# Optimization experiments

Measured on AMD Instinct MI355X. Metric: run time of the kernel, lower is better.

Reference implementation:

```python
import jax, jax.numpy as jnp
import numpy as np


def setup_inputs() -> dict:
    N, E, D = 50000, 800000, 64
    key = jax.random.key(0)
    ks = jax.random.split(key, 8)
    s = 1.0 / np.sqrt(2 * D)
    inp = {
        "node_emb": jax.random.normal(ks[0], (N, D), dtype=jnp.float32),
        "edge_index": jax.random.randint(ks[1], (2, E), 0, N, dtype=jnp.int64),
        "W1": jax.random.normal(ks[2], (2 * D, D), dtype=jnp.float32) * s,
        "b1": jnp.zeros((D,), dtype=jnp.float32),
        "W2": jax.random.normal(ks[3], (D, D), dtype=jnp.float32) * (1.0 / np.sqrt(D)),
        "b2": jnp.zeros((D,), dtype=jnp.float32),
        "Wg": jax.random.normal(ks[4], (D, D), dtype=jnp.float32) * (1.0 / np.sqrt(D)),
        "bg": jnp.zeros((D,), dtype=jnp.float32),
    }
    return inp


def reference(node_emb, edge_index, W1, b1, W2, b2, Wg, bg):
    # Gather pairwise embeddings along edges
    src, dst = edge_index[0], edge_index[1]
    pair_emb = jnp.concatenate([node_emb[src], node_emb[dst]], axis=-1)  # [E, 2D]
    # Interaction MLP (dropout in eval mode -> identity)
    h = jax.nn.relu(pair_emb @ W1 + b1)
    interaction = h @ W2 + b2  # [E, D]
    # Sigmoid gate
    gate = jax.nn.sigmoid(interaction @ Wg + bg)
    gated = interaction * gate  # [E, D]
    # Scatter-mean back to source nodes
    N = node_emb.shape[0]
    summed = jax.ops.segment_sum(gated, src, num_segments=N)  # [N, D]
    counts = jax.ops.segment_sum(jnp.ones((src.shape[0],), dtype=gated.dtype), src, num_segments=N)
    pooled = summed / jnp.maximum(counts, 1.0)[:, None]
    return pooled
```

## Files before the change

kernel.cpp:

```cpp
#include <hip/hip_runtime.h>


typedef unsigned short ushort_t;
typedef __attribute__((ext_vector_type(8))) short     bf16x8;
typedef __attribute__((ext_vector_type(8))) unsigned short u16x8;
typedef __attribute__((ext_vector_type(4))) float     f32x4;

constexpr int D        = 64;
constexpr int TILE     = 64;
constexpr int BLOCK    = 256;
constexpr int NFRAG    = 32;
constexpr int SLAB_B   = 4352;
constexpr int PAIR_STR = 136;
constexpr int H_STR    = 72;

static __device__ __forceinline__ ushort_t f2bf(float f) {
    union { float f; unsigned int u; } v; v.f = f;
    const unsigned int r = v.u + 0x7FFFu + ((v.u >> 16) & 1u);
    return (ushort_t)(r >> 16);
}


__global__ void prep_kernel(const float* __restrict__ W1, const float* __restrict__ W2,
                            const float* __restrict__ Wg,
                            const float* __restrict__ b2, const float* __restrict__ bg,
                            const float* __restrict__ emb, const int* __restrict__ ei,
                            ushort_t* __restrict__ wpack, float* __restrict__ bgp,
                            ushort_t* __restrict__ emb_bf, int* __restrict__ cnt,
                            float* __restrict__ summed,
                            int total_emb, int cvt_blocks, int e4blocks, int E) {
    const int bid = blockIdx.x;
    if (bid < 64) {
        const int t = bid * 256 + threadIdx.x;
        const int f = t >> 9;
        const int l = (t >> 3) & 63;
        const int j = t & 7;
        const int k = ((f < 16) ? (f & 3) : ((f - 16) & 1)) * 32 + (l >> 4) * 8 + j;
        const int n = ((f < 16) ? (f >> 2) : (((f & 7)) >> 1)) * 16 + (l & 15);
        float v;
        if (f < 16)      v = W1[k * 64 + n];
        else if (f < 24) v = W2[k * 64 + n];
        else {
            float s = 0.f;
            const float* wr = W2 + k * 64;
#pragma unroll 8
            for (int m = 0; m < 64; ++m) s += wr[m] * Wg[m * 64 + n];
            v = s;
        }
        wpack[t] = f2bf(v);
    } else if (bid < 64 + cvt_blocks) {
        const int idx  = (bid - 64) * 256 + threadIdx.x;
        const int base = idx * 8;
        if (base < total_emb) {
            const float4 a = *(const float4*)(emb + base);
            const float4 b = *(const float4*)(emb + base + 4);
            u16x8 p;
            p[0]=f2bf(a.x); p[1]=f2bf(a.y); p[2]=f2bf(a.z); p[3]=f2bf(a.w);
            p[4]=f2bf(b.x); p[5]=f2bf(b.y); p[6]=f2bf(b.z); p[7]=f2bf(b.w);
            *(u16x8*)(emb_bf + base) = p;
        }
    } else if (bid == 64 + cvt_blocks) {
        const int n = threadIdx.x;
        if (n < 64) {
            float s = bg[n];
#pragma unroll 8
            for (int m = 0; m < 64; ++m) s += b2[m] * Wg[m * 64 + n];
            bgp[n] = s;
        }
    } else if (bid < 65 + cvt_blocks + e4blocks) {
        const int e = ((bid - 65 - cvt_blocks) * 256 + threadIdx.x) * 4;
        if (e + 3 < E) {
            const int4 v = *(const int4*)(ei + e);
            atomicAdd(&cnt[v.x], 1); atomicAdd(&cnt[v.y], 1);
            atomicAdd(&cnt[v.z], 1); atomicAdd(&cnt[v.w], 1);
        } else {
            for (int k = e; k < E; ++k) atomicAdd(&cnt[ei[k]], 1);
        }
    } else {
        const int idx  = (bid - 65 - cvt_blocks - e4blocks) * 256 + threadIdx.x;
        const int base = idx * 4;
        if (base < total_emb)
            *(float4*)(summed + base) = (float4){0.f, 0.f, 0.f, 0.f};
    }
}


__global__ void scan_block(const int* __restrict__ cnt, int* __restrict__ off,
                           int* __restrict__ bsum, int N) {
    __shared__ int s[256];
    const int t = threadIdx.x, i = blockIdx.x * 256 + t;
    const int x = (i < N) ? cnt[i] : 0;
    s[t] = x; __syncthreads();
    for (int d = 1; d < 256; d <<= 1) {
        const int v = (t >= d) ? s[t - d] : 0;
        __syncthreads();
        s[t] += v;
        __syncthreads();
    }
    if (i < N) off[i] = s[t] - x;
    if (t == 255) bsum[blockIdx.x] = s[255];
}

__global__ void scatter_idx(const int* __restrict__ ei, int* __restrict__ off,
                            const int* __restrict__ bsum, unsigned* __restrict__ sorted,
                            int E, int nb) {
    __shared__ int pref[256];
    const int t = threadIdx.x;
    const int x = (t < nb) ? bsum[t] : 0;
    pref[t] = x; __syncthreads();
    for (int d = 1; d < 256; d <<= 1) {
        const int v = (t >= d) ? pref[t - d] : 0;
        __syncthreads();
        pref[t] += v;
        __syncthreads();
    }
    const int e = (blockIdx.x * blockDim.x + t) * 4;
    if (e + 3 < E) {
        const int4 v = *(const int4*)(ei + e);
        const int4 d = *(const int4*)(ei + E + e);
        const int bx = v.x >> 8, by = v.y >> 8, bz = v.z >> 8, bw = v.w >> 8;
        sorted[(bx ? pref[bx - 1] : 0) + atomicAdd(&off[v.x], 1)] =
            ((unsigned)v.x << 16) | (unsigned)d.x;
        sorted[(by ? pref[by - 1] : 0) + atomicAdd(&off[v.y], 1)] =
            ((unsigned)v.y << 16) | (unsigned)d.y;
        sorted[(bz ? pref[bz - 1] : 0) + atomicAdd(&off[v.z], 1)] =
            ((unsigned)v.z << 16) | (unsigned)d.z;
        sorted[(bw ? pref[bw - 1] : 0) + atomicAdd(&off[v.w], 1)] =
            ((unsigned)v.w << 16) | (unsigned)d.w;
    } else {
        for (int k = e; k < E; ++k) {
            const int s = ei[k], b = s >> 8;
            sorted[(b ? pref[b - 1] : 0) + atomicAdd(&off[s], 1)] =
                ((unsigned)s << 16) | (unsigned)ei[E + k];
        }
    }
}


__global__ __launch_bounds__(BLOCK, 8)
void edge_mlp_mfma(const ushort_t* __restrict__ emb_bf,
                   const unsigned* __restrict__ sorted,
                   const ushort_t* __restrict__ wpack,
                   const float* __restrict__ b1, const float* __restrict__ b2,
                   const float* __restrict__ bgp,
                   const int*   __restrict__ cnt,
                   float* __restrict__ summed,
                   int E)
{
    __shared__ char  slab[4][SLAB_B];
    __shared__ int   srcIds[TILE];
    __shared__ float rcS[TILE];

    const int tid = threadIdx.x;

    {
        const int e = tid >> 2, q4 = tid & 3;
        ushort_t* prow = (ushort_t*)&slab[e >> 4][(e & 15) * (PAIR_STR * 2)];
        const int ide = blockIdx.x * TILE + e;
        if (ide < E) {
            const unsigned p = sorted[ide];
            const int s  = (int)(p >> 16);
            const int dn = (int)(p & 0xFFFFu);
            if (q4 == 0) { srcIds[e] = s; rcS[e] = 1.0f / fmaxf((float)cnt[s], 1.0f); }
            const ushort_t* sr = emb_bf + (size_t)s  * D + q4 * 16;
            const ushort_t* dr = emb_bf + (size_t)dn * D + q4 * 16;
            *(u16x8*)&prow[q4 * 16]          = *(const u16x8*)sr;
            *(u16x8*)&prow[q4 * 16 + 8]      = *(const u16x8*)(sr + 8);
            *(u16x8*)&prow[64 + q4 * 16]     = *(const u16x8*)dr;
            *(u16x8*)&prow[64 + q4 * 16 + 8] = *(const u16x8*)(dr + 8);
        } else {
            if (q4 == 0) { srcIds[e] = -1; rcS[e] = 1.0f; }
            const u16x8 z = {0,0,0,0,0,0,0,0};
            *(u16x8*)&prow[q4 * 16]          = z;
            *(u16x8*)&prow[q4 * 16 + 8]      = z;
            *(u16x8*)&prow[64 + q4 * 16]     = z;
            *(u16x8*)&prow[64 + q4 * 16 + 8] = z;
        }
    }

    const int w    = tid >> 6;
    const int ln   = tid & 63;
    const int quad = ln >> 4;
    const int cn   = ln & 15;
    ushort_t* pairW = (ushort_t*)slab[w];
    ushort_t* hW    = (ushort_t*)slab[w];

    f32x4 acc1[4];
#pragma unroll
    for (int nt = 0; nt < 4; ++nt) {
        const float b = b1[nt * 16 + cn];
        acc1[nt] = (f32x4){b, b, b, b};
    }
#pragma unroll
    for (int kc = 0; kc < 4; ++kc) {
        const bf16x8 a = *(const bf16x8*)&pairW[cn * PAIR_STR + kc * 32 + quad * 8];
#pragma unroll
        for (int nt = 0; nt < 4; ++nt) {
            const bf16x8 bf = *(const bf16x8*)(wpack + ((nt * 4 + kc) * 64 + ln) * 8);
            acc1[nt] = __builtin_amdgcn_mfma_f32_16x16x32_bf16(a, bf, acc1[nt], 0, 0, 0);
        }
    }
#pragma unroll
    for (int nt = 0; nt < 4; ++nt)
#pragma unroll
        for (int r = 0; r < 4; ++r)
            hW[(quad * 4 + r) * H_STR + nt * 16 + cn] = f2bf(fmaxf(acc1[nt][r], 0.f));

    f32x4 acc2[4], accg[4];
#pragma unroll
    for (int nt = 0; nt < 4; ++nt) {
        const float b  = b2 [nt * 16 + cn];
        const float bG = bgp[nt * 16 + cn];
        acc2[nt] = (f32x4){b, b, b, b};
        accg[nt] = (f32x4){bG, bG, bG, bG};
    }
#pragma unroll
    for (int kc = 0; kc < 2; ++kc) {
        const bf16x8 a = *(const bf16x8*)&hW[cn * H_STR + kc * 32 + quad * 8];
#pragma unroll
        for (int nt = 0; nt < 4; ++nt) {
            const bf16x8 bf2 = *(const bf16x8*)(wpack + ((16 + nt * 2 + kc) * 64 + ln) * 8);
            const bf16x8 bfg = *(const bf16x8*)(wpack + ((24 + nt * 2 + kc) * 64 + ln) * 8);
            acc2[nt] = __builtin_amdgcn_mfma_f32_16x16x32_bf16(a, bf2, acc2[nt], 0, 0, 0);
            accg[nt] = __builtin_amdgcn_mfma_f32_16x16x32_bf16(a, bfg, accg[nt], 0, 0, 0);
        }
    }

    float g[4][4];
#pragma unroll
    for (int nt = 0; nt < 4; ++nt)
#pragma unroll
        for (int r = 0; r < 4; ++r)
            g[nt][r] = acc2[nt][r] / (1.0f + __expf(-accg[nt][r]));

    {
        const int rbase = 16 * w;
        float part0 = 0.f, part1 = 0.f, part2 = 0.f, part3 = 0.f;
        int   segSrc = srcIds[rbase];
        int   segRow = 0;
#pragma unroll
        for (int i = 0; i < 16; ++i) {
            const int s = srcIds[rbase + i];
            if (s != segSrc) {
                if (segSrc >= 0) {
                    float t0 = part0, t1 = part1, t2 = part2, t3 = part3;
                    t0 += __shfl_xor(t0, 16); t0 += __shfl_xor(t0, 32);
                    t1 += __shfl_xor(t1, 16); t1 += __shfl_xor(t1, 32);
                    t2 += __shfl_xor(t2, 16); t2 += __shfl_xor(t2, 32);
                    t3 += __shfl_xor(t3, 16); t3 += __shfl_xor(t3, 32);
                    const float tot = (quad < 2) ? (quad == 0 ? t0 : t1)
                                                 : (quad == 2 ? t2 : t3);
                    unsafeAtomicAdd(&summed[(size_t)segSrc * D + ln],
                                    tot * rcS[rbase + segRow]);
                }
                part0 = part1 = part2 = part3 = 0.f;
                segSrc = s;
                segRow = i;
            }
            if ((i >> 2) == quad) {
                part0 += g[0][i & 3];
                part1 += g[1][i & 3];
                part2 += g[2][i & 3];
                part3 += g[3][i & 3];
            }
        }
        if (segSrc >= 0) {
            float t0 = part0, t1 = part1, t2 = part2, t3 = part3;
            t0 += __shfl_xor(t0, 16); t0 += __shfl_xor(t0, 32);
            t1 += __shfl_xor(t1, 16); t1 += __shfl_xor(t1, 32);
            t2 += __shfl_xor(t2, 16); t2 += __shfl_xor(t2, 32);
            t3 += __shfl_xor(t3, 16); t3 += __shfl_xor(t3, 32);
            const float tot = (quad < 2) ? (quad == 0 ? t0 : t1)
                                         : (quad == 2 ? t2 : t3);
            unsafeAtomicAdd(&summed[(size_t)segSrc * D + ln],
                            tot * rcS[rbase + segRow]);
        }
    }
}

extern "C" void kernel_launch(void* const* d_in, const int* in_sizes, int n_in,
                              void* d_out, int out_size, void* d_ws, size_t ws_size,
                              hipStream_t stream) {
    const float* node_emb   = (const float*)d_in[0];
    const int*   edge_index = (const int*)d_in[1];
    const float* W1 = (const float*)d_in[2];
    const float* b1 = (const float*)d_in[3];
    const float* W2 = (const float*)d_in[4];
    const float* b2 = (const float*)d_in[5];
    const float* Wg = (const float*)d_in[6];
    const float* bg = (const float*)d_in[7];

    const int N = in_sizes[0] / D;
    const int E = in_sizes[1] / 2;
    const int total_emb = N * D;

    int* cnt    = (int*)d_ws;
    int* off    = cnt + N;
    int* bsum   = off + N;
    unsigned* sorted = (unsigned*)(bsum + 256);
    float* bgp  = (float*)(sorted + E);
    ushort_t* wpack  = (ushort_t*)(bgp + 64);
    ushort_t* emb_bf = wpack + NFRAG * 512;

    float* summed = (float*)d_out;

    hipMemsetAsync(cnt, 0, sizeof(int) * (size_t)N, stream);

    const int cvt_blocks = (total_emb / 8 + 255) / 256;
    const int e4blocks   = ((E + 3) / 4 + 255) / 256;
    const int zblocks    = (total_emb / 4 + 255) / 256;
    prep_kernel<<<64 + cvt_blocks + 1 + e4blocks + zblocks, 256, 0, stream>>>(
        W1, W2, Wg, b2, bg, node_emb, edge_index,
        wpack, bgp, emb_bf, cnt, summed, total_emb, cvt_blocks, e4blocks, E);

    const int nblocks = (N + 255) / 256;
    scan_block <<<nblocks, 256, 0, stream>>>(cnt, off, bsum, N);
    scatter_idx<<<e4blocks, 256, 0, stream>>>(edge_index, off, bsum, sorted, E, nblocks);

    const int ntiles = (E + TILE - 1) / TILE;
    edge_mlp_mfma<<<ntiles, BLOCK, 0, stream>>>(emb_bf, sorted, wpack,
                                                b1, b2, bgp, cnt, summed, E);
}
```

Measured before the change: 245.3 us.

## Fuse all stages into one persistent kernel with software grid barriers

Merges the prep, counting, scan, scatter and edge-MLP kernels into a single persistent kernel of 1024 blocks. The stages are separated by atomic-counter grid barriers, and the MFMA tiles are processed in a grid-stride loop. The aim is to remove kernel launch gaps and the separate memset of the counts. The cost is spin-wait barriers, which deadlock if not all blocks are co-resident, reduced parallelism in the fill phases, and lower occupancy from launch_bounds 4.

```diff
diff --git a/kernel.cpp b/kernel.cpp
--- a/kernel.cpp
+++ b/kernel.cpp
@@ -9,6 +9,7 @@
 constexpr int D        = 64;
 constexpr int TILE     = 64;
 constexpr int BLOCK    = 256;
+constexpr int NBLK     = 1024;
 constexpr int NFRAG    = 32;
 constexpr int SLAB_B   = 4352;
 constexpr int PAIR_STR = 136;
@@ -20,18 +21,39 @@
     return (ushort_t)(r >> 16);
 }
 
-
-__global__ void prep_kernel(const float* __restrict__ W1, const float* __restrict__ W2,
-                            const float* __restrict__ Wg,
-                            const float* __restrict__ b2, const float* __restrict__ bg,
-                            const float* __restrict__ emb, const int* __restrict__ ei,
-                            ushort_t* __restrict__ wpack, float* __restrict__ bgp,
-                            ushort_t* __restrict__ emb_bf, int* __restrict__ cnt,
-                            float* __restrict__ summed,
-                            int total_emb, int cvt_blocks, int e4blocks, int E) {
+static __device__ __forceinline__ void grid_sync(unsigned* bar, unsigned target) {
+    __syncthreads();
+    if (threadIdx.x == 0) {
+        __hip_atomic_fetch_add(bar, 1u, __ATOMIC_ACQ_REL, __HIP_MEMORY_SCOPE_AGENT);
+        while (__hip_atomic_load(bar, __ATOMIC_ACQUIRE, __HIP_MEMORY_SCOPE_AGENT) < target)
+            __builtin_amdgcn_s_sleep(8);
+    }
+    __syncthreads();
+}
+
+__global__ __launch_bounds__(BLOCK, 4)
+void uber_kernel(const float* __restrict__ W1, const float* __restrict__ W2,
+                 const float* __restrict__ Wg, const float* __restrict__ pb1,
+                 const float* __restrict__ pb2, const float* __restrict__ pbg,
+                 const float* __restrict__ emb, const int* __restrict__ ei,
+                 unsigned* __restrict__ bar, int* __restrict__ cnt,
+                 int* __restrict__ off, int* __restrict__ bsum,
+                 unsigned* __restrict__ sorted, float* __restrict__ bgp,
+                 ushort_t* __restrict__ wpack, ushort_t* __restrict__ emb_bf,
+                 float* __restrict__ summed,
+                 int N, int E, int total_emb, int ntiles, int nsb)
+{
+    __shared__ char  slab[4][SLAB_B];
+    __shared__ int   si[256];
+    __shared__ int   srcIds[TILE];
+    __shared__ float rcS[TILE];
+
+    const int tid = threadIdx.x;
     const int bid = blockIdx.x;
-    if (bid < 64) {
-        const int t = bid * 256 + threadIdx.x;
+    const int gid = bid * BLOCK + tid;
+    constexpr int G = NBLK * BLOCK;
+
+    for (int t = gid; t < NFRAG * 512; t += G) {
         const int f = t >> 9;
         const int l = (t >> 3) & 63;
         const int j = t & 7;
@@ -48,27 +70,30 @@
             v = s;
         }
         wpack[t] = f2bf(v);
-    } else if (bid < 64 + cvt_blocks) {
-        const int idx  = (bid - 64) * 256 + threadIdx.x;
-        const int base = idx * 8;
-        if (base < total_emb) {
-            const float4 a = *(const float4*)(emb + base);
-            const float4 b = *(const float4*)(emb + base + 4);
-            u16x8 p;
-            p[0]=f2bf(a.x); p[1]=f2bf(a.y); p[2]=f2bf(a.z); p[3]=f2bf(a.w);
-            p[4]=f2bf(b.x); p[5]=f2bf(b.y); p[6]=f2bf(b.z); p[7]=f2bf(b.w);
-            *(u16x8*)(emb_bf + base) = p;
-        }
-    } else if (bid == 64 + cvt_blocks) {
-        const int n = threadIdx.x;
-        if (n < 64) {
-            float s = bg[n];
+    }
+    if (gid < 64) {
+        float s = pbg[gid];
 #pragma unroll 8
-            for (int m = 0; m < 64; ++m) s += b2[m] * Wg[m * 64 + n];
-            bgp[n] = s;
-        }
-    } else if (bid < 65 + cvt_blocks + e4blocks) {
-        const int e = ((bid - 65 - cvt_blocks) * 256 + threadIdx.x) * 4;
+        for (int m = 0; m < 64; ++m) s += pb2[m] * Wg[m * 64 + gid];
+        bgp[gid] = s;
+    }
+    for (int i = gid; i < N; i += G) cnt[i] = 0;
+    for (int i = gid; i * 8 < total_emb; i += G) {
+        const int base = i * 8;
+        const float4 a = *(const float4*)(emb + base);
+        const float4 b = *(const float4*)(emb + base + 4);
+        u16x8 p;
+        p[0]=f2bf(a.x); p[1]=f2bf(a.y); p[2]=f2bf(a.z); p[3]=f2bf(a.w);
+        p[4]=f2bf(b.x); p[5]=f2bf(b.y); p[6]=f2bf(b.z); p[7]=f2bf(b.w);
+        *(u16x8*)(emb_bf + base) = p;
+    }
+    for (int i = gid; i * 4 < total_emb; i += G)
+        *(float4*)(summed + i * 4) = (float4){0.f, 0.f, 0.f, 0.f};
+
+    grid_sync(bar, 1u * NBLK);
+
+    for (int i = gid; i * 4 < E; i += G) {
+        const int e = i * 4;
         if (e + 3 < E) {
             const int4 v = *(const int4*)(ei + e);
             atomicAdd(&cnt[v.x], 1); atomicAdd(&cnt[v.y], 1);
@@ -76,107 +101,59 @@
         } else {
             for (int k = e; k < E; ++k) atomicAdd(&cnt[ei[k]], 1);
         }
-    } else {
-        const int idx  = (bid - 65 - cvt_blocks - e4blocks) * 256 + threadIdx.x;
-        const int base = idx * 4;
-        if (base < total_emb)
-            *(float4*)(summed + base) = (float4){0.f, 0.f, 0.f, 0.f};
-    }
-}
-
-
-__global__ void scan_block(const int* __restrict__ cnt, int* __restrict__ off,
-                           int* __restrict__ bsum, int N) {
-    __shared__ int s[256];
-    const int t = threadIdx.x, i = blockIdx.x * 256 + t;
-    const int x = (i < N) ? cnt[i] : 0;
-    s[t] = x; __syncthreads();
-    for (int d = 1; d < 256; d <<= 1) {
-        const int v = (t >= d) ? s[t - d] : 0;
-        __syncthreads();
-        s[t] += v;
-        __syncthreads();
-    }
-    if (i < N) off[i] = s[t] - x;
-    if (t == 255) bsum[blockIdx.x] = s[255];
-}
-
-__global__ void scatter_idx(const int* __restrict__ ei, int* __restrict__ off,
-                            const int* __restrict__ bsum, unsigned* __restrict__ sorted,
-                            int E, int nb) {
-    __shared__ int pref[256];
-    const int t = threadIdx.x;
-    const int x = (t < nb) ? bsum[t] : 0;
-    pref[t] = x; __syncthreads();
-    for (int d = 1; d < 256; d <<= 1) {
-        const int v = (t >= d) ? pref[t - d] : 0;
-        __syncthreads();
-        pref[t] += v;
-        __syncthreads();
-    }
-    const int e = (blockIdx.x * blockDim.x + t) * 4;
-    if (e + 3 < E) {
-        const int4 v = *(const int4*)(ei + e);
-        const int4 d = *(const int4*)(ei + E + e);
-        const int bx = v.x >> 8, by = v.y >> 8, bz = v.z >> 8, bw = v.w >> 8;
-        sorted[(bx ? pref[bx - 1] : 0) + atomicAdd(&off[v.x], 1)] =
-            ((unsigned)v.x << 16) | (unsigned)d.x;
-        sorted[(by ? pref[by - 1] : 0) + atomicAdd(&off[v.y], 1)] =
-            ((unsigned)v.y << 16) | (unsigned)d.y;
-        sorted[(bz ? pref[bz - 1] : 0) + atomicAdd(&off[v.z], 1)] =
-            ((unsigned)v.z << 16) | (unsigned)d.z;
-        sorted[(bw ? pref[bw - 1] : 0) + atomicAdd(&off[v.w], 1)] =
-            ((unsigned)v.w << 16) | (unsigned)d.w;
-    } else {
-        for (int k = e; k < E; ++k) {
-            const int s = ei[k], b = s >> 8;
-            sorted[(b ? pref[b - 1] : 0) + atomicAdd(&off[s], 1)] =
-                ((unsigned)s << 16) | (unsigned)ei[E + k];
-        }
-    }
-}
-
-
-__global__ __launch_bounds__(BLOCK, 8)
-void edge_mlp_mfma(const ushort_t* __restrict__ emb_bf,
-                   const unsigned* __restrict__ sorted,
-                   const ushort_t* __restrict__ wpack,
-                   const float* __restrict__ b1, const float* __restrict__ b2,
-                   const float* __restrict__ bgp,
-                   const int*   __restrict__ cnt,
-                   float* __restrict__ summed,
-                   int E)
-{
-    __shared__ char  slab[4][SLAB_B];
-    __shared__ int   srcIds[TILE];
-    __shared__ float rcS[TILE];
-
-    const int tid = threadIdx.x;
-
-    {
-        const int e = tid >> 2, q4 = tid & 3;
-        ushort_t* prow = (ushort_t*)&slab[e >> 4][(e & 15) * (PAIR_STR * 2)];
-        const int ide = blockIdx.x * TILE + e;
-        if (ide < E) {
-            const unsigned p = sorted[ide];
-            const int s  = (int)(p >> 16);
-            const int dn = (int)(p & 0xFFFFu);
-            if (q4 == 0) { srcIds[e] = s; rcS[e] = 1.0f / fmaxf((float)cnt[s], 1.0f); }
-            const ushort_t* sr = emb_bf + (size_t)s  * D + q4 * 16;
-            const ushort_t* dr = emb_bf + (size_t)dn * D + q4 * 16;
-            *(u16x8*)&prow[q4 * 16]          = *(const u16x8*)sr;
-            *(u16x8*)&prow[q4 * 16 + 8]      = *(const u16x8*)(sr + 8);
-            *(u16x8*)&prow[64 + q4 * 16]     = *(const u16x8*)dr;
-            *(u16x8*)&prow[64 + q4 * 16 + 8] = *(const u16x8*)(dr + 8);
+    }
+    grid_sync(bar, 2u * NBLK);
+
+    if (bid < nsb) {
+        const int i = bid * 256 + tid;
+        const int x = (i < N) ? cnt[i] : 0;
+        si[tid] = x; __syncthreads();
+        for (int d = 1; d < 256; d <<= 1) {
+            const int v = (tid >= d) ? si[tid - d] : 0;
+            __syncthreads();
+            si[tid] += v;
+            __syncthreads();
+        }
+        if (i < N) off[i] = si[tid] - x;
+        if (tid == 255) bsum[bid] = si[255];
+    }
+    grid_sync(bar, 3u * NBLK);
+
+    if (bid == 0) {
+        const int x = (tid < nsb) ? bsum[tid] : 0;
+        si[tid] = x; __syncthreads();
+        for (int d = 1; d < 256; d <<= 1) {
+            const int v = (tid >= d) ? si[tid - d] : 0;
+            __syncthreads();
+            si[tid] += v;
+            __syncthreads();
+        }
+        if (tid < nsb) bsum[tid] = si[tid] - x;
+    }
+    grid_sync(bar, 4u * NBLK);
+
+    for (int i = gid; i * 4 < E; i += G) {
+        const int e = i * 4;
+        if (e + 3 < E) {
+            const int4 v  = *(const int4*)(ei + e);
+            const int4 d4 = *(const int4*)(ei + E + e);
+            sorted[bsum[v.x >> 8] + atomicAdd(&off[v.x], 1)] =
+                ((unsigned)v.x << 16) | (unsigned)d4.x;
+            sorted[bsum[v.y >> 8] + atomicAdd(&off[v.y], 1)] =
+                ((unsigned)v.y << 16) | (unsigned)d4.y;
+            sorted[bsum[v.z >> 8] + atomicAdd(&off[v.z], 1)] =
+                ((unsigned)v.z << 16) | (unsigned)d4.z;
+            sorted[bsum[v.w >> 8] + atomicAdd(&off[v.w], 1)] =
+                ((unsigned)v.w << 16) | (unsigned)d4.w;
         } else {
-            if (q4 == 0) { srcIds[e] = -1; rcS[e] = 1.0f; }
-            const u16x8 z = {0,0,0,0,0,0,0,0};
-            *(u16x8*)&prow[q4 * 16]          = z;
-            *(u16x8*)&prow[q4 * 16 + 8]      = z;
-            *(u16x8*)&prow[64 + q4 * 16]     = z;
-            *(u16x8*)&prow[64 + q4 * 16 + 8] = z;
-        }
-    }
+            for (int k = e; k < E; ++k) {
+                const int s = ei[k];
+                sorted[bsum[s >> 8] + atomicAdd(&off[s], 1)] =
+                    ((unsigned)s << 16) | (unsigned)ei[E + k];
+            }
+        }
+    }
+    grid_sync(bar, 5u * NBLK);
 
     const int w    = tid >> 6;
     const int ln   = tid & 63;
@@ -185,95 +162,122 @@
     ushort_t* pairW = (ushort_t*)slab[w];
     ushort_t* hW    = (ushort_t*)slab[w];
 
-    f32x4 acc1[4];
-#pragma unroll
-    for (int nt = 0; nt < 4; ++nt) {
-        const float b = b1[nt * 16 + cn];
-        acc1[nt] = (f32x4){b, b, b, b};
-    }
-#pragma unroll
-    for (int kc = 0; kc < 4; ++kc) {
-        const bf16x8 a = *(const bf16x8*)&pairW[cn * PAIR_STR + kc * 32 + quad * 8];
+    for (int tile = bid; tile < ntiles; tile += NBLK) {
+        {
+            const int e = tid >> 2, q4 = tid & 3;
+            ushort_t* prow = (ushort_t*)&slab[e >> 4][(e & 15) * (PAIR_STR * 2)];
+            const int ide = tile * TILE + e;
+            if (ide < E) {
+                const unsigned p = sorted[ide];
+                const int s  = (int)(p >> 16);
+                const int dn = (int)(p & 0xFFFFu);
+                if (q4 == 0) { srcIds[e] = s; rcS[e] = 1.0f / fmaxf((float)cnt[s], 1.0f); }
+                const ushort_t* sr = emb_bf + (size_t)s  * D + q4 * 16;
+                const ushort_t* dr = emb_bf + (size_t)dn * D + q4 * 16;
+                *(u16x8*)&prow[q4 * 16]          = *(const u16x8*)sr;
+                *(u16x8*)&prow[q4 * 16 + 8]      = *(const u16x8*)(sr + 8);
+                *(u16x8*)&prow[64 + q4 * 16]     = *(const u16x8*)dr;
+                *(u16x8*)&prow[64 + q4 * 16 + 8] = *(const u16x8*)(dr + 8);
+            } else {
+                if (q4 == 0) { srcIds[e] = -1; rcS[e] = 1.0f; }
+                const u16x8 z = {0,0,0,0,0,0,0,0};
+                *(u16x8*)&prow[q4 * 16]          = z;
+                *(u16x8*)&prow[q4 * 16 + 8]      = z;
+                *(u16x8*)&prow[64 + q4 * 16]     = z;
+                *(u16x8*)&prow[64 + q4 * 16 + 8] = z;
+            }
+        }
+
+        f32x4 acc1[4];
 #pragma unroll
         for (int nt = 0; nt < 4; ++nt) {
-            const bf16x8 bf = *(const bf16x8*)(wpack + ((nt * 4 + kc) * 64 + ln) * 8);
-            acc1[nt] = __builtin_amdgcn_mfma_f32_16x16x32_bf16(a, bf, acc1[nt], 0, 0, 0);
-        }
-    }
-#pragma unroll
-    for (int nt = 0; nt < 4; ++nt)
-#pragma unroll
-        for (int r = 0; r < 4; ++r)
-            hW[(quad * 4 + r) * H_STR + nt * 16 + cn] = f2bf(fmaxf(acc1[nt][r], 0.f));
-
-    f32x4 acc2[4], accg[4];
-#pragma unroll
-    for (int nt = 0; nt < 4; ++nt) {
-        const float b  = b2 [nt * 16 + cn];
-        const float bG = bgp[nt * 16 + cn];
-        acc2[nt] = (f32x4){b, b, b, b};
-        accg[nt] = (f32x4){bG, bG, bG, bG};
-    }
-#pragma unroll
-    for (int kc = 0; kc < 2; ++kc) {
-        const bf16x8 a = *(const bf16x8*)&hW[cn * H_STR + kc * 32 + quad * 8];
+            const float b = pb1[nt * 16 + cn];
+            acc1[nt] = (f32x4){b, b, b, b};
+        }
+#pragma unroll
+        for (int kc = 0; kc < 4; ++kc) {
+            const bf16x8 a = *(const bf16x8*)&pairW[cn * PAIR_STR + kc * 32 + quad * 8];
+#pragma unroll
+            for (int nt = 0; nt < 4; ++nt) {
+                const bf16x8 bf = *(const bf16x8*)(wpack + ((nt * 4 + kc) * 64 + ln) * 8);
+                acc1[nt] = __builtin_amdgcn_mfma_f32_16x16x32_bf16(a, bf, acc1[nt], 0, 0, 0);
+            }
+        }
+#pragma unroll
+        for (int nt = 0; nt < 4; ++nt)
+#pragma unroll
+            for (int r = 0; r < 4; ++r)
+                hW[(quad * 4 + r) * H_STR + nt * 16 + cn] = f2bf(fmaxf(acc1[nt][r], 0.f));
+
+        f32x4 acc2[4], accg[4];
 #pragma unroll
         for (int nt = 0; nt < 4; ++nt) {
-            const bf16x8 bf2 = *(const bf16x8*)(wpack + ((16 + nt * 2 + kc) * 64 + ln) * 8);
-            const bf16x8 bfg = *(const bf16x8*)(wpack + ((24 + nt * 2 + kc) * 64 + ln) * 8);
-            acc2[nt] = __builtin_amdgcn_mfma_f32_16x16x32_bf16(a, bf2, acc2[nt], 0, 0, 0);
-            accg[nt] = __builtin_amdgcn_mfma_f32_16x16x32_bf16(a, bfg, accg[nt], 0, 0, 0);
-        }
-    }
-
-    float g[4][4];
-#pragma unroll
-    for (int nt = 0; nt < 4; ++nt)
-#pragma unroll
-        for (int r = 0; r < 4; ++r)
-            g[nt][r] = acc2[nt][r] / (1.0f + __expf(-accg[nt][r]));
-
-    {
-        const int rbase = 16 * w;
-        float part0 = 0.f, part1 = 0.f, part2 = 0.f, part3 = 0.f;
-        int   segSrc = srcIds[rbase];
-        int   segRow = 0;
-#pragma unroll
-        for (int i = 0; i < 16; ++i) {
-            const int s = srcIds[rbase + i];
-            if (s != segSrc) {
-                if (segSrc >= 0) {
-                    float t0 = part0, t1 = part1, t2 = part2, t3 = part3;
-                    t0 += __shfl_xor(t0, 16); t0 += __shfl_xor(t0, 32);
-                    t1 += __shfl_xor(t1, 16); t1 += __shfl_xor(t1, 32);
-                    t2 += __shfl_xor(t2, 16); t2 += __shfl_xor(t2, 32);
-                    t3 += __shfl_xor(t3, 16); t3 += __shfl_xor(t3, 32);
-                    const float tot = (quad < 2) ? (quad == 0 ? t0 : t1)
-                                                 : (quad == 2 ? t2 : t3);
-                    unsafeAtomicAdd(&summed[(size_t)segSrc * D + ln],
-                                    tot * rcS[rbase + segRow]);
+            const float b  = pb2[nt * 16 + cn];
+            const float bG = bgp[nt * 16 + cn];
+            acc2[nt] = (f32x4){b, b, b, b};
+            accg[nt] = (f32x4){bG, bG, bG, bG};
+        }
+#pragma unroll
+        for (int kc = 0; kc < 2; ++kc) {
+            const bf16x8 a = *(const bf16x8*)&hW[cn * H_STR + kc * 32 + quad * 8];
+#pragma unroll
+            for (int nt = 0; nt < 4; ++nt) {
+                const bf16x8 bf2 = *(const bf16x8*)(wpack + ((16 + nt * 2 + kc) * 64 + ln) * 8);
+                const bf16x8 bfg = *(const bf16x8*)(wpack + ((24 + nt * 2 + kc) * 64 + ln) * 8);
+                acc2[nt] = __builtin_amdgcn_mfma_f32_16x16x32_bf16(a, bf2, acc2[nt], 0, 0, 0);
+                accg[nt] = __builtin_amdgcn_mfma_f32_16x16x32_bf16(a, bfg, accg[nt], 0, 0, 0);
+            }
+        }
+
+        float g[4][4];
+#pragma unroll
+        for (int nt = 0; nt < 4; ++nt)
+#pragma unroll
+            for (int r = 0; r < 4; ++r)
+                g[nt][r] = acc2[nt][r] / (1.0f + __expf(-accg[nt][r]));
+
+        {
+            const int rbase = 16 * w;
+            float part0 = 0.f, part1 = 0.f, part2 = 0.f, part3 = 0.f;
+            int   segSrc = srcIds[rbase];
+            int   segRow = 0;
+#pragma unroll
+            for (int i = 0; i < 16; ++i) {
+                const int s = srcIds[rbase + i];
+                if (s != segSrc) {
+                    if (segSrc >= 0) {
+                        float t0 = part0, t1 = part1, t2 = part2, t3 = part3;
+                        t0 += __shfl_xor(t0, 16); t0 += __shfl_xor(t0, 32);
+                        t1 += __shfl_xor(t1, 16); t1 += __shfl_xor(t1, 32);
+                        t2 += __shfl_xor(t2, 16); t2 += __shfl_xor(t2, 32);
+                        t3 += __shfl_xor(t3, 16); t3 += __shfl_xor(t3, 32);
+                        const float tot = (quad < 2) ? (quad == 0 ? t0 : t1)
+                                                     : (quad == 2 ? t2 : t3);
+                        unsafeAtomicAdd(&summed[(size_t)segSrc * D + ln],
+                                        tot * rcS[rbase + segRow]);
+                    }
+                    part0 = part1 = part2 = part3 = 0.f;
+                    segSrc = s;
+                    segRow = i;
                 }
-                part0 = part1 = part2 = part3 = 0.f;
-                segSrc = s;
-                segRow = i;
-            }
-            if ((i >> 2) == quad) {
-                part0 += g[0][i & 3];
-                part1 += g[1][i & 3];
-                part2 += g[2][i & 3];
-                part3 += g[3][i & 3];
-            }
-        }
-        if (segSrc >= 0) {
-            float t0 = part0, t1 = part1, t2 = part2, t3 = part3;
-            t0 += __shfl_xor(t0, 16); t0 += __shfl_xor(t0, 32);
-            t1 += __shfl_xor(t1, 16); t1 += __shfl_xor(t1, 32);
-            t2 += __shfl_xor(t2, 16); t2 += __shfl_xor(t2, 32);
-            t3 += __shfl_xor(t3, 16); t3 += __shfl_xor(t3, 32);
-            const float tot = (quad < 2) ? (quad == 0 ? t0 : t1)
-                                         : (quad == 2 ? t2 : t3);
-            unsafeAtomicAdd(&summed[(size_t)segSrc * D + ln],
-                            tot * rcS[rbase + segRow]);
+                if ((i >> 2) == quad) {
+                    part0 += g[0][i & 3];
+                    part1 += g[1][i & 3];
+                    part2 += g[2][i & 3];
+                    part3 += g[3][i & 3];
+                }
+            }
+            if (segSrc >= 0) {
+                float t0 = part0, t1 = part1, t2 = part2, t3 = part3;
+                t0 += __shfl_xor(t0, 16); t0 += __shfl_xor(t0, 32);
+                t1 += __shfl_xor(t1, 16); t1 += __shfl_xor(t1, 32);
+                t2 += __shfl_xor(t2, 16); t2 += __shfl_xor(t2, 32);
+                t3 += __shfl_xor(t3, 16); t3 += __shfl_xor(t3, 32);
+                const float tot = (quad < 2) ? (quad == 0 ? t0 : t1)
+                                             : (quad == 2 ? t2 : t3);
+                unsafeAtomicAdd(&summed[(size_t)segSrc * D + ln],
+                                tot * rcS[rbase + segRow]);
+            }
         }
     }
 }
@@ -294,30 +298,23 @@
     const int E = in_sizes[1] / 2;
     const int total_emb = N * D;
 
-    int* cnt    = (int*)d_ws;
+    unsigned* bar = (unsigned*)d_ws;
+    int* cnt    = (int*)d_ws + 16;
     int* off    = cnt + N;
     int* bsum   = off + N;
-    unsigned* sorted = (unsigned*)(bsum + 256);
+    unsigned* sorted = (unsigned*)(bsum + 240);
     float* bgp  = (float*)(sorted + E);
     ushort_t* wpack  = (ushort_t*)(bgp + 64);
     ushort_t* emb_bf = wpack + NFRAG * 512;
 
     float* summed = (float*)d_out;
 
-    hipMemsetAsync(cnt, 0, sizeof(int) * (size_t)N, stream);
-
-    const int cvt_blocks = (total_emb / 8 + 255) / 256;
-    const int e4blocks   = ((E + 3) / 4 + 255) / 256;
-    const int zblocks    = (total_emb / 4 + 255) / 256;
-    prep_kernel<<<64 + cvt_blocks + 1 + e4blocks + zblocks, 256, 0, stream>>>(
-        W1, W2, Wg, b2, bg, node_emb, edge_index,
-        wpack, bgp, emb_bf, cnt, summed, total_emb, cvt_blocks, e4blocks, E);
-
-    const int nblocks = (N + 255) / 256;
-    scan_block <<<nblocks, 256, 0, stream>>>(cnt, off, bsum, N);
-    scatter_idx<<<e4blocks, 256, 0, stream>>>(edge_index, off, bsum, sorted, E, nblocks);
+    hipMemsetAsync(bar, 0, 64, stream);
 
     const int ntiles = (E + TILE - 1) / TILE;
-    edge_mlp_mfma<<<ntiles, BLOCK, 0, stream>>>(emb_bf, sorted, wpack,
-                                                b1, b2, bgp, cnt, summed, E);
+    const int nsb    = (N + 255) / 256;
+    uber_kernel<<<NBLK, BLOCK, 0, stream>>>(
+        W1, W2, Wg, b1, b2, bg, node_emb, edge_index,
+        bar, cnt, off, bsum, sorted, bgp, wpack, emb_bf,
+        summed, N, E, total_emb, ntiles, nsb);
 }
```

New measurement: 850.0 us. +246.6%, slower.

## Make edge MLP kernel persistent with register prefetch of next tile's gathers

Applied to the files above, without the earlier changes.

The edge MLP kernel becomes a grid-stride persistent kernel with a fixed grid of 1536 blocks, each looping over many 64-edge tiles. Inside the loop, the sorted-index lookup and bf16 embedding gathers for the next tile are issued into registers after the first MFMA stage, so their global-memory latency overlaps the remaining matmuls and the scatter of the current tile. Occupancy hint drops from 8 to 6 blocks to make room for the prefetch registers. The trade-off is fewer resident waves to hide latency, plus possible tail imbalance from the fixed grid.

```diff
diff --git a/kernel.cpp b/kernel.cpp
--- a/kernel.cpp
+++ b/kernel.cpp
@@ -9,6 +9,7 @@
 constexpr int D        = 64;
 constexpr int TILE     = 64;
 constexpr int BLOCK    = 256;
+constexpr int NBLK_M   = 1536;
 constexpr int NFRAG    = 32;
 constexpr int SLAB_B   = 4352;
 constexpr int PAIR_STR = 136;
@@ -116,28 +117,28 @@
     }
     const int e = (blockIdx.x * blockDim.x + t) * 4;
     if (e + 3 < E) {
-        const int4 v = *(const int4*)(ei + e);
-        const int4 d = *(const int4*)(ei + E + e);
+        const int4 v  = *(const int4*)(ei + e);
+        const int4 d4 = *(const int4*)(ei + E + e);
         const int bx = v.x >> 8, by = v.y >> 8, bz = v.z >> 8, bw = v.w >> 8;
         sorted[(bx ? pref[bx - 1] : 0) + atomicAdd(&off[v.x], 1)] =
-            ((unsigned)v.x << 16) | (unsigned)d.x;
+            ((unsigned)v.x << 16) | (unsigned)d4.x;
         sorted[(by ? pref[by - 1] : 0) + atomicAdd(&off[v.y], 1)] =
-            ((unsigned)v.y << 16) | (unsigned)d.y;
+            ((unsigned)v.y << 16) | (unsigned)d4.y;
         sorted[(bz ? pref[bz - 1] : 0) + atomicAdd(&off[v.z], 1)] =
-            ((unsigned)v.z << 16) | (unsigned)d.z;
+            ((unsigned)v.z << 16) | (unsigned)d4.z;
         sorted[(bw ? pref[bw - 1] : 0) + atomicAdd(&off[v.w], 1)] =
-            ((unsigned)v.w << 16) | (unsigned)d.w;
+            ((unsigned)v.w << 16) | (unsigned)d4.w;
     } else {
         for (int k = e; k < E; ++k) {
-            const int s = ei[k], b = s >> 8;
-            sorted[(b ? pref[b - 1] : 0) + atomicAdd(&off[s], 1)] =
+            const int s = ei[k], c = s >> 8;
+            sorted[(c ? pref[c - 1] : 0) + atomicAdd(&off[s], 1)] =
                 ((unsigned)s << 16) | (unsigned)ei[E + k];
         }
     }
 }
 
 
-__global__ __launch_bounds__(BLOCK, 8)
+__global__ __launch_bounds__(BLOCK, 6)
 void edge_mlp_mfma(const ushort_t* __restrict__ emb_bf,
                    const unsigned* __restrict__ sorted,
                    const ushort_t* __restrict__ wpack,
@@ -145,135 +146,159 @@
                    const float* __restrict__ bgp,
                    const int*   __restrict__ cnt,
                    float* __restrict__ summed,
-                   int E)
+                   int E, int ntiles)
 {
     __shared__ char  slab[4][SLAB_B];
     __shared__ int   srcIds[TILE];
     __shared__ float rcS[TILE];
 
-    const int tid = threadIdx.x;
-
-    {
-        const int e = tid >> 2, q4 = tid & 3;
-        ushort_t* prow = (ushort_t*)&slab[e >> 4][(e & 15) * (PAIR_STR * 2)];
-        const int ide = blockIdx.x * TILE + e;
-        if (ide < E) {
-            const unsigned p = sorted[ide];
-            const int s  = (int)(p >> 16);
-            const int dn = (int)(p & 0xFFFFu);
-            if (q4 == 0) { srcIds[e] = s; rcS[e] = 1.0f / fmaxf((float)cnt[s], 1.0f); }
-            const ushort_t* sr = emb_bf + (size_t)s  * D + q4 * 16;
-            const ushort_t* dr = emb_bf + (size_t)dn * D + q4 * 16;
-            *(u16x8*)&prow[q4 * 16]          = *(const u16x8*)sr;
-            *(u16x8*)&prow[q4 * 16 + 8]      = *(const u16x8*)(sr + 8);
-            *(u16x8*)&prow[64 + q4 * 16]     = *(const u16x8*)dr;
-            *(u16x8*)&prow[64 + q4 * 16 + 8] = *(const u16x8*)(dr + 8);
-        } else {
-            if (q4 == 0) { srcIds[e] = -1; rcS[e] = 1.0f; }
-            const u16x8 z = {0,0,0,0,0,0,0,0};
-            *(u16x8*)&prow[q4 * 16]          = z;
-            *(u16x8*)&prow[q4 * 16 + 8]      = z;
-            *(u16x8*)&prow[64 + q4 * 16]     = z;
-            *(u16x8*)&prow[64 + q4 * 16 + 8] = z;
-        }
-    }
-
+    const int tid  = threadIdx.x;
+    const int e    = tid >> 2, q4 = tid & 3;
     const int w    = tid >> 6;
     const int ln   = tid & 63;
     const int quad = ln >> 4;
     const int cn   = ln & 15;
+    ushort_t* prow  = (ushort_t*)&slab[e >> 4][(e & 15) * (PAIR_STR * 2)];
     ushort_t* pairW = (ushort_t*)slab[w];
     ushort_t* hW    = (ushort_t*)slab[w];
 
-    f32x4 acc1[4];
-#pragma unroll
-    for (int nt = 0; nt < 4; ++nt) {
-        const float b = b1[nt * 16 + cn];
-        acc1[nt] = (f32x4){b, b, b, b};
-    }
-#pragma unroll
-    for (int kc = 0; kc < 4; ++kc) {
-        const bf16x8 a = *(const bf16x8*)&pairW[cn * PAIR_STR + kc * 32 + quad * 8];
+    const u16x8 z = {0,0,0,0,0,0,0,0};
+    u16x8 r0 = z, r1 = z, r2 = z, r3 = z;
+    int   ps  = -1;
+    float prc = 1.0f;
+
+    {
+        const int ide = blockIdx.x * TILE + e;
+        if (blockIdx.x < ntiles && ide < E) {
+            const unsigned p = sorted[ide];
+            const int s  = (int)(p >> 16);
+            const int dn = (int)(p & 0xFFFFu);
+            ps = s;
+            if (q4 == 0) prc = 1.0f / fmaxf((float)cnt[s], 1.0f);
+            const ushort_t* sr = emb_bf + (size_t)s  * D + q4 * 16;
+            const ushort_t* dr = emb_bf + (size_t)dn * D + q4 * 16;
+            r0 = *(const u16x8*)sr; r1 = *(const u16x8*)(sr + 8);
+            r2 = *(const u16x8*)dr; r3 = *(const u16x8*)(dr + 8);
+        }
+    }
+
+    for (int tile = blockIdx.x; tile < ntiles; tile += gridDim.x) {
+        *(u16x8*)&prow[q4 * 16]          = r0;
+        *(u16x8*)&prow[q4 * 16 + 8]      = r1;
+        *(u16x8*)&prow[64 + q4 * 16]     = r2;
+        *(u16x8*)&prow[64 + q4 * 16 + 8] = r3;
+        if (q4 == 0) { srcIds[e] = ps; rcS[e] = prc; }
+
+        f32x4 acc1[4];
 #pragma unroll
         for (int nt = 0; nt < 4; ++nt) {
-            const bf16x8 bf = *(const bf16x8*)(wpack + ((nt * 4 + kc) * 64 + ln) * 8);
-            acc1[nt] = __builtin_amdgcn_mfma_f32_16x16x32_bf16(a, bf, acc1[nt], 0, 0, 0);
-        }
-    }
-#pragma unroll
-    for (int nt = 0; nt < 4; ++nt)
-#pragma unroll
-        for (int r = 0; r < 4; ++r)
-            hW[(quad * 4 + r) * H_STR + nt * 16 + cn] = f2bf(fmaxf(acc1[nt][r], 0.f));
-
-    f32x4 acc2[4], accg[4];
-#pragma unroll
-    for (int nt = 0; nt < 4; ++nt) {
-        const float b  = b2 [nt * 16 + cn];
-        const float bG = bgp[nt * 16 + cn];
-        acc2[nt] = (f32x4){b, b, b, b};
-        accg[nt] = (f32x4){bG, bG, bG, bG};
-    }
-#pragma unroll
-    for (int kc = 0; kc < 2; ++kc) {
-        const bf16x8 a = *(const bf16x8*)&hW[cn * H_STR + kc * 32 + quad * 8];
+            const float b = b1[nt * 16 + cn];
+            acc1[nt] = (f32x4){b, b, b, b};
+        }
+#pragma unroll
+        for (int kc = 0; kc < 4; ++kc) {
+            const bf16x8 a = *(const bf16x8*)&pairW[cn * PAIR_STR + kc * 32 + quad * 8];
+#pragma unroll
+            for (int nt = 0; nt < 4; ++nt) {
+                const bf16x8 bf = *(const bf16x8*)(wpack + ((nt * 4 + kc) * 64 + ln) * 8);
+                acc1[nt] = __builtin_amdgcn_mfma_f32_16x16x32_bf16(a, bf, acc1[nt], 0, 0, 0);
+            }
+        }
+
+        {
+            const int t2  = tile + (int)gridDim.x;
+            const int ide = t2 * TILE + e;
+            if (t2 < ntiles && ide < E) {
+                const unsigned p = sorted[ide];
+                const int s  = (int)(p >> 16);
+                const int dn = (int)(p & 0xFFFFu);
+                ps = s;
+                if (q4 == 0) prc = 1.0f / fmaxf((float)cnt[s], 1.0f);
+                const ushort_t* sr = emb_bf + (size_t)s  * D + q4 * 16;
+                const ushort_t* dr = emb_bf + (size_t)dn * D + q4 * 16;
+                r0 = *(const u16x8*)sr; r1 = *(const u16x8*)(sr + 8);
+                r2 = *(const u16x8*)dr; r3 = *(const u16x8*)(dr + 8);
+            } else {
+                ps = -1; prc = 1.0f;
+                r0 = z; r1 = z; r2 = z; r3 = z;
+            }
+        }
+
+#pragma unroll
+        for (int nt = 0; nt < 4; ++nt)
+#pragma unroll
+            for (int r = 0; r < 4; ++r)
+                hW[(quad * 4 + r) * H_STR + nt * 16 + cn] = f2bf(fmaxf(acc1[nt][r], 0.f));
+
+        f32x4 acc2[4], accg[4];
 #pragma unroll
         for (int nt = 0; nt < 4; ++nt) {
-            const bf16x8 bf2 = *(const bf16x8*)(wpack + ((16 + nt * 2 + kc) * 64 + ln) * 8);
-            const bf16x8 bfg = *(const bf16x8*)(wpack + ((24 + nt * 2 + kc) * 64 + ln) * 8);
-            acc2[nt] = __builtin_amdgcn_mfma_f32_16x16x32_bf16(a, bf2, acc2[nt], 0, 0, 0);
-            accg[nt] = __builtin_amdgcn_mfma_f32_16x16x32_bf16(a, bfg, accg[nt], 0, 0, 0);
-        }
-    }
-
-    float g[4][4];
-#pragma unroll
-    for (int nt = 0; nt < 4; ++nt)
-#pragma unroll
-        for (int r = 0; r < 4; ++r)
-            g[nt][r] = acc2[nt][r] / (1.0f + __expf(-accg[nt][r]));
-
-    {
-        const int rbase = 16 * w;
-        float part0 = 0.f, part1 = 0.f, part2 = 0.f, part3 = 0.f;
-        int   segSrc = srcIds[rbase];
-        int   segRow = 0;
-#pragma unroll
-        for (int i = 0; i < 16; ++i) {
-            const int s = srcIds[rbase + i];
-            if (s != segSrc) {
-                if (segSrc >= 0) {
-                    float t0 = part0, t1 = part1, t2 = part2, t3 = part3;
-                    t0 += __shfl_xor(t0, 16); t0 += __shfl_xor(t0, 32);
-                    t1 += __shfl_xor(t1, 16); t1 += __shfl_xor(t1, 32);
-                    t2 += __shfl_xor(t2, 16); t2 += __shfl_xor(t2, 32);
-                    t3 += __shfl_xor(t3, 16); t3 += __shfl_xor(t3, 32);
-                    const float tot = (quad < 2) ? (quad == 0 ? t0 : t1)
-                                                 : (quad == 2 ? t2 : t3);
-                    unsafeAtomicAdd(&summed[(size_t)segSrc * D + ln],
-                                    tot * rcS[rbase + segRow]);
+            const float b  = b2 [nt * 16 + cn];
+            const float bG = bgp[nt * 16 + cn];
+            acc2[nt] = (f32x4){b, b, b, b};
+            accg[nt] = (f32x4){bG, bG, bG, bG};
+        }
+#pragma unroll
+        for (int kc = 0; kc < 2; ++kc) {
+            const bf16x8 a = *(const bf16x8*)&hW[cn * H_STR + kc * 32 + quad * 8];
+#pragma unroll
+            for (int nt = 0; nt < 4; ++nt) {
+                const bf16x8 bf2 = *(const bf16x8*)(wpack + ((16 + nt * 2 + kc) * 64 + ln) * 8);
+                const bf16x8 bfg = *(const bf16x8*)(wpack + ((24 + nt * 2 + kc) * 64 + ln) * 8);
+                acc2[nt] = __builtin_amdgcn_mfma_f32_16x16x32_bf16(a, bf2, acc2[nt], 0, 0, 0);
+                accg[nt] = __builtin_amdgcn_mfma_f32_16x16x32_bf16(a, bfg, accg[nt], 0, 0, 0);
+            }
+        }
+
+        float g[4][4];
+#pragma unroll
+        for (int nt = 0; nt < 4; ++nt)
+#pragma unroll
+            for (int r = 0; r < 4; ++r)
+                g[nt][r] = acc2[nt][r] / (1.0f + __expf(-accg[nt][r]));
+
+        {
+            const int rbase = 16 * w;
+            float part0 = 0.f, part1 = 0.f, part2 = 0.f, part3 = 0.f;
+            int   segSrc = srcIds[rbase];
+            int   segRow = 0;
+#pragma unroll
+            for (int i = 0; i < 16; ++i) {
+                const int s = srcIds[rbase + i];
+                if (s != segSrc) {
+                    if (segSrc >= 0) {
+                        float t0 = part0, t1 = part1, t2 = part2, t3 = part3;
+                        t0 += __shfl_xor(t0, 16); t0 += __shfl_xor(t0, 32);
+                        t1 += __shfl_xor(t1, 16); t1 += __shfl_xor(t1, 32);
+                        t2 += __shfl_xor(t2, 16); t2 += __shfl_xor(t2, 32);
+                        t3 += __shfl_xor(t3, 16); t3 += __shfl_xor(t3, 32);
+                        const float tot = (quad < 2) ? (quad == 0 ? t0 : t1)
+                                                     : (quad == 2 ? t2 : t3);
+                        unsafeAtomicAdd(&summed[(size_t)segSrc * D + ln],
+                                        tot * rcS[rbase + segRow]);
+                    }
+                    part0 = part1 = part2 = part3 = 0.f;
+                    segSrc = s;
+                    segRow = i;
                 }
-                part0 = part1 = part2 = part3 = 0.f;
-                segSrc = s;
-                segRow = i;
-            }
-            if ((i >> 2) == quad) {
-                part0 += g[0][i & 3];
-                part1 += g[1][i & 3];
-                part2 += g[2][i & 3];
-                part3 += g[3][i & 3];
-            }
-        }
-        if (segSrc >= 0) {
-            float t0 = part0, t1 = part1, t2 = part2, t3 = part3;
-            t0 += __shfl_xor(t0, 16); t0 += __shfl_xor(t0, 32);
-            t1 += __shfl_xor(t1, 16); t1 += __shfl_xor(t1, 32);
-            t2 += __shfl_xor(t2, 16); t2 += __shfl_xor(t2, 32);
-            t3 += __shfl_xor(t3, 16); t3 += __shfl_xor(t3, 32);
-            const float tot = (quad < 2) ? (quad == 0 ? t0 : t1)
-                                         : (quad == 2 ? t2 : t3);
-            unsafeAtomicAdd(&summed[(size_t)segSrc * D + ln],
-                            tot * rcS[rbase + segRow]);
+                if ((i >> 2) == quad) {
+                    part0 += g[0][i & 3];
+                    part1 += g[1][i & 3];
+                    part2 += g[2][i & 3];
+                    part3 += g[3][i & 3];
+                }
+            }
+            if (segSrc >= 0) {
+                float t0 = part0, t1 = part1, t2 = part2, t3 = part3;
+                t0 += __shfl_xor(t0, 16); t0 += __shfl_xor(t0, 32);
+                t1 += __shfl_xor(t1, 16); t1 += __shfl_xor(t1, 32);
+                t2 += __shfl_xor(t2, 16); t2 += __shfl_xor(t2, 32);
+                t3 += __shfl_xor(t3, 16); t3 += __shfl_xor(t3, 32);
+                const float tot = (quad < 2) ? (quad == 0 ? t0 : t1)
+                                             : (quad == 2 ? t2 : t3);
+                unsafeAtomicAdd(&summed[(size_t)segSrc * D + ln],
+                                tot * rcS[rbase + segRow]);
+            }
         }
     }
 }
@@ -318,6 +343,6 @@
     scatter_idx<<<e4blocks, 256, 0, stream>>>(edge_index, off, bsum, sorted, E, nblocks);
 
     const int ntiles = (E + TILE - 1) / TILE;
-    edge_mlp_mfma<<<ntiles, BLOCK, 0, stream>>>(emb_bf, sorted, wpack,
-                                                b1, b2, bgp, cnt, summed, E);
-}
+    edge_mlp_mfma<<<NBLK_M, BLOCK, 0, stream>>>(emb_bf, sorted, wpack,
+                                                b1, b2, bgp, cnt, summed, E, ntiles);
+}
```

Result: slower. 656.5 us (+167.7%).
